# Kernel optimization log

Hardware: AMD Instinct MI355X
Metric: run time of the kernel (lower is better)

Reference implementation:

```python
import jax, jax.numpy as jnp
import numpy as np

EPS = 1e-6
ROPE_THETA = 10000.0


def setup_inputs() -> dict:
    key = jax.random.key(0)
    ks = jax.random.split(key, 6)
    B, S, D = 2, 2048, 2048
    H, KVH, HD = 16, 4, 128
    hidden_states = jax.random.normal(ks[0], (B, S, D), dtype=jnp.float32)
    # RoPE tables (HF style: freqs duplicated across the two halves)
    inv_freq = 1.0 / (ROPE_THETA ** (jnp.arange(0, HD, 2, dtype=jnp.float32) / HD))
    pos = jnp.arange(S, dtype=jnp.float32)
    freqs = pos[:, None] * inv_freq[None, :]            # [S, HD/2]
    emb = jnp.concatenate([freqs, freqs], axis=-1)       # [S, HD]
    cos, sin = jnp.cos(emb), jnp.sin(emb)
    w_scale = 0.02
    q_w = jax.random.normal(ks[1], (H * HD, D), dtype=jnp.float32) * w_scale
    k_w = jax.random.normal(ks[2], (KVH * HD, D), dtype=jnp.float32) * w_scale
    v_w = jax.random.normal(ks[3], (KVH * HD, D), dtype=jnp.float32) * w_scale
    o_w = jax.random.normal(ks[4], (D, H * HD), dtype=jnp.float32) * w_scale
    q_norm_w = jnp.ones((HD,), dtype=jnp.float32)
    k_norm_w = jnp.ones((HD,), dtype=jnp.float32)
    return {
        "hidden_states": hidden_states, "cos": cos, "sin": sin,
        "q_w": q_w, "k_w": k_w, "v_w": v_w, "o_w": o_w,
        "q_norm_w": q_norm_w, "k_norm_w": k_norm_w,
    }


def _rms_norm(x, w):
    # Qwen3RMSNorm: fp32 variance, scale, cast back
    xf = x.astype(jnp.float32)
    var = jnp.mean(xf * xf, axis=-1, keepdims=True)
    out = xf * jax.lax.rsqrt(var + EPS)
    return (out * w.astype(jnp.float32)).astype(x.dtype)


def _rotate_half(x):
    half = x.shape[-1] // 2
    return jnp.concatenate([-x[..., half:], x[..., :half]], axis=-1)


def reference(hidden_states, cos, sin, q_w, k_w, v_w, o_w, q_norm_w, k_norm_w):
    B, S, D = hidden_states.shape
    HD = q_norm_w.shape[0]
    H = q_w.shape[0] // HD
    KVH = k_w.shape[0] // HD
    groups = H // KVH
    scale = HD ** -0.5

    # QKV projections (no bias) -> [B, heads, S, HD]
    q = (hidden_states @ q_w.T).reshape(B, S, H, HD)
    k = (hidden_states @ k_w.T).reshape(B, S, KVH, HD)
    v = (hidden_states @ v_w.T).reshape(B, S, KVH, HD)
    q = _rms_norm(q, q_norm_w).transpose(0, 2, 1, 3)   # [B,H,S,HD]
    k = _rms_norm(k, k_norm_w).transpose(0, 2, 1, 3)   # [B,KVH,S,HD]
    v = v.transpose(0, 2, 1, 3)                        # [B,KVH,S,HD]

    # RoPE (broadcast over batch and heads)
    c = cos[None, None, :, :]
    s = sin[None, None, :, :]
    q = q * c + _rotate_half(q) * s
    k = k * c + _rotate_half(k) * s

    # GQA expand kv heads
    if groups > 1:
        k = jnp.repeat(k, groups, axis=1)              # [B,H,S,HD]
        v = jnp.repeat(v, groups, axis=1)

    # SDPA, non-causal, no mask, no dropout
    scores = jnp.einsum("bhqd,bhkd->bhqk", q, k) * scale
    probs = jax.nn.softmax(scores, axis=-1)
    attn = jnp.einsum("bhqk,bhkd->bhqd", probs, v)     # [B,H,S,HD]

    attn = attn.transpose(0, 2, 1, 3).reshape(B, S, H * HD)
    return attn @ o_w.T
```

## Files before the change

kernel.cpp:

```cpp
#include <hip/hip_runtime.h>
#include <hip/hip_bf16.h>
#include <math.h>

#define B_   2
#define S_   2048
#define D_   2048
#define H_   16
#define KVH_ 4
#define HD_  128
#define SCALE 0.08838834764831845f
#define LOG2E 1.44269504088896f
#define EPS_  1e-6f

typedef unsigned short u16;
typedef unsigned int   u32;
typedef __attribute__((ext_vector_type(2)))  unsigned int u32x2;
typedef __attribute__((ext_vector_type(8)))  short bf16x8;
typedef __attribute__((ext_vector_type(4)))  float f32x4;
typedef __attribute__((ext_vector_type(16))) float f32x16;

__device__ __forceinline__ u16 f2bf(float x) {
    union { float f; unsigned int u; } v; v.f = x;
    unsigned int r = v.u + 0x7fffu + ((v.u >> 16) & 1u);
    return (u16)(r >> 16);
}
__device__ __forceinline__ float bf2f(u16 b) {
    union { float f; unsigned int u; } v; v.u = ((unsigned int)b) << 16;
    return v.f;
}
__device__ __forceinline__ u32 cvtpk(float lo, float hi) {
    u32 r;
    asm("v_cvt_pk_bf16_f32 %0, %1, %2" : "=v"(r) : "v"(lo), "v"(hi));
    return r;
}
__device__ __forceinline__ void gload16(const void* g, void* lds) {
    __builtin_amdgcn_global_load_lds(
        (const __attribute__((address_space(1))) unsigned int*)g,
        (__attribute__((address_space(3))) unsigned int*)lds, 16, 0, 0);
}

__global__ __launch_bounds__(256) void f2b_all(
    const float* __restrict__ s0, u16* __restrict__ d0, int n0,
    const float* __restrict__ s1, u16* __restrict__ d1, int n1,
    const float* __restrict__ s2, u16* __restrict__ d2, int n2,
    const float* __restrict__ s3, u16* __restrict__ d3, int n3,
    const float* __restrict__ s4, u16* __restrict__ d4, int n4)
{
    const float* s; u16* d; int n;
    switch (blockIdx.y) {
        case 0: s = s0; d = d0; n = n0; break;
        case 1: s = s1; d = d1; n = n1; break;
        case 2: s = s2; d = d2; n = n2; break;
        case 3: s = s3; d = d3; n = n3; break;
        default: s = s4; d = d4; n = n4; break;
    }
    int i = blockIdx.x * 256 + threadIdx.x;
    if (i >= n) return;
    float4 v = ((const float4*)s)[i];
    ushort4 o = make_ushort4(f2bf(v.x), f2bf(v.y), f2bf(v.z), f2bf(v.w));
    ((ushort4*)d)[i] = o;
}

template<int MODE>
__global__ __launch_bounds__(256) void gemm_bf16(
    const u16* __restrict__ A,
    const u16* __restrict__ Bw,
    u16* __restrict__ Qo, u16* __restrict__ Ko, u16* __restrict__ Vt,
    float* __restrict__ Co)
{
    __shared__ u16 As[128 * 64];
    __shared__ u16 Bs[128 * 64];

    const int t  = threadIdx.x;
    const int w  = t >> 6, l = t & 63;
    const int wm = w >> 1, wn = w & 1;
    const int lr = l & 15, lh = l >> 4;
    const int n0 = blockIdx.x * 128;
    const int m0 = blockIdx.y * 128;

    f32x4 acc[4][4];
    #pragma unroll
    for (int i = 0; i < 4; ++i)
        #pragma unroll
        for (int j = 0; j < 4; ++j)
            acc[i][j] = (f32x4)0.f;

    const int x = (w * 4) * 1024 + l * 16;
    for (int k0 = 0; k0 < 2048; k0 += 64) {
        #pragma unroll
        for (int u = 0; u < 4; ++u) {
            int xb = x + u * 1024;
            int r  = xb >> 7;
            int c  = xb & 127;
            int cs = c ^ ((r & 7) << 4);
            gload16(&A[(size_t)(m0 + r) * 2048 + k0 + (cs >> 1)], &As[(w * 4 + u) * 512]);
            gload16(&Bw[(size_t)(n0 + r) * 2048 + k0 + (cs >> 1)], &Bs[(w * 4 + u) * 512]);
        }
        __syncthreads();
        #pragma unroll
        for (int kc = 0; kc < 2; ++kc) {
            bf16x8 af[4], bfr[4];
            #pragma unroll
            for (int i = 0; i < 4; ++i) {
                int row = wm * 64 + i * 16 + lr;
                int byt = row * 128 + ((kc * 64 + lh * 16) ^ ((row & 7) << 4));
                af[i] = *(const bf16x8*)&As[byt >> 1];
                int rob = wn * 64 + i * 16 + lr;
                int byb = rob * 128 + ((kc * 64 + lh * 16) ^ ((rob & 7) << 4));
                bfr[i] = *(const bf16x8*)&Bs[byb >> 1];
            }
            #pragma unroll
            for (int i = 0; i < 4; ++i)
                #pragma unroll
                for (int j = 0; j < 4; ++j)
                    acc[i][j] = __builtin_amdgcn_mfma_f32_16x16x32_bf16(
                        af[i], bfr[j], acc[i][j], 0, 0, 0);
        }
        __syncthreads();
    }

    #pragma unroll
    for (int i = 0; i < 4; ++i) {
        #pragma unroll
        for (int j = 0; j < 4; ++j) {
            int col = n0 + wn * 64 + j * 16 + lr;
            #pragma unroll
            for (int r = 0; r < 4; ++r) {
                int m = m0 + wm * 64 + i * 16 + lh * 4 + r;
                float v = acc[i][j][r];
                if (MODE == 0) {
                    int bb = m >> 11, s = m & 2047;
                    if (col < 2048) {
                        int hh = col >> 7, d = col & 127;
                        Qo[((size_t)(bb * H_ + hh) * S_ + s) * HD_ + d] = f2bf(v);
                    } else if (col < 2560) {
                        int c2 = col - 2048; int hh = c2 >> 7, d = c2 & 127;
                        Ko[((size_t)(bb * KVH_ + hh) * S_ + s) * HD_ + d] = f2bf(v);
                    } else {
                        int c2 = col - 2560; int hh = c2 >> 7, d = c2 & 127;
                        Vt[((size_t)(bb * KVH_ + hh) * HD_ + d) * S_ + s] = f2bf(v);
                    }
                } else {
                    Co[(size_t)m * 2048 + col] = v;
                }
            }
        }
    }
}

__global__ __launch_bounds__(256) void norm_rope(
    u16* __restrict__ Qb, u16* __restrict__ Kb,
    const float* __restrict__ cosb, const float* __restrict__ sinb,
    const float* __restrict__ qnw, const float* __restrict__ knw)
{
    const int rid = blockIdx.x * 4 + (threadIdx.x >> 6);
    const int l   = threadIdx.x & 63;
    u16* row; const float* wn; int s; float sc;
    if (rid < B_ * H_ * S_) {
        row = Qb + (size_t)rid * HD_; wn = qnw; s = rid & (S_ - 1); sc = SCALE * LOG2E;
    } else {
        int r2 = rid - B_ * H_ * S_;
        row = Kb + (size_t)r2 * HD_; wn = knw; s = r2 & (S_ - 1); sc = 1.f;
    }
    unsigned int u = *(const unsigned int*)&row[2 * l];
    float x0 = bf2f((u16)(u & 0xffff)), x1 = bf2f((u16)(u >> 16));
    float ss = x0 * x0 + x1 * x1;
    #pragma unroll
    for (int off = 1; off < 64; off <<= 1) ss += __shfl_xor(ss, off);
    float rr = rsqrtf(ss * (1.f / 128.f) + 1e-6f);
    float n0 = x0 * rr * wn[2 * l];
    float n1 = x1 * rr * wn[2 * l + 1];
    float p0 = __shfl_xor(n0, 32);
    float p1 = __shfl_xor(n1, 32);
    float sg = (l < 32) ? -1.f : 1.f;
    const float* cp = cosb + s * HD_;
    const float* sp = sinb + s * HD_;
    float o0 = (n0 * cp[2 * l]     + sg * p0 * sp[2 * l])     * sc;
    float o1 = (n1 * cp[2 * l + 1] + sg * p1 * sp[2 * l + 1]) * sc;
    unsigned int o = (unsigned int)f2bf(o0) | ((unsigned int)f2bf(o1) << 16);
    *(unsigned int*)&row[2 * l] = o;
}

__global__ __launch_bounds__(256, 2) void attn_mfma(
    const u16* __restrict__ Q,
    const u16* __restrict__ K,
    const u16* __restrict__ Vt,
    u16* __restrict__ AO)
{
    __shared__ u16 Ks[2][64 * 128];
    __shared__ u16 Vs[3][128 * 64];

    const int t  = threadIdx.x, w = t >> 6, l = t & 63;
    const int lq = l & 31, hi = l >> 5;
    const int id = (blockIdx.x & 7) * 64 + (blockIdx.x >> 3);
    const int qx = id & 15, bh = id >> 4;
    const int bb = bh >> 4, h = bh & 15;
    const int kv = bb * KVH_ + (h >> 2);
    const int q0 = qx * 128 + w * 32;

    const u16* Qp = Q + ((size_t)bh * S_ + q0) * HD_;
    const u16* Kp = K + (size_t)kv * S_ * HD_;
    const u16* Vp = Vt + (size_t)kv * HD_ * S_;

    bf16x8 aq[8];
    #pragma unroll
    for (int ks = 0; ks < 8; ++ks)
        aq[ks] = *(const bf16x8*)&Qp[(size_t)lq * 128 + ks * 16 + hi * 8];

    f32x16 oacc[4];
    #pragma unroll
    for (int dt = 0; dt < 4; ++dt) oacc[dt] = (f32x16)0.f;
    float mrun = -1e30f, lrun = 0.f;
    u32 pan[16];

    auto stage = [&](int k0, int kbuf, int vbuf) {
        #pragma unroll
        for (int u = 0; u < 4; ++u) {
            int xb = (w * 4 + u) * 1024 + l * 16;
            int rk = xb >> 8, ck = xb & 255;
            gload16(&Kp[(size_t)(k0 + rk) * 128 + ((ck ^ ((rk & 7) << 4)) >> 1)],
                    &Ks[kbuf][(w * 4 + u) * 512]);
            int rv = xb >> 7, cv = xb & 127;
            gload16(&Vp[(size_t)rv * S_ + k0 + ((cv ^ ((rv & 7) << 4)) >> 1)],
                    &Vs[vbuf][(w * 4 + u) * 512]);
        }
    };

    stage(0, 0, 0);
    __syncthreads();

    const int NT = S_ / 64;
    for (int kt = 0; kt < NT; ++kt) {
        const int kcur = kt & 1;
        if (kt + 1 < NT) stage((kt + 1) * 64, (kt + 1) & 1, (kt + 1) % 3);

        f32x16 sacc[2];
        sacc[0] = (f32x16)0.f; sacc[1] = (f32x16)0.f;
        #pragma unroll
        for (int kb = 0; kb < 2; ++kb) {
            #pragma unroll
            for (int ks = 0; ks < 8; ++ks) {
                int row = kb * 32 + lq;
                int byt = row * 256 + ((ks * 32 + hi * 16) ^ ((row & 7) << 4));
                bf16x8 kf = *(const bf16x8*)&Ks[kcur][byt >> 1];
                sacc[kb] = __builtin_amdgcn_mfma_f32_32x32x16_bf16(
                    kf, aq[ks], sacc[kb], 0, 0, 0);
            }
        }

        float mx = -1e30f;
        #pragma unroll
        for (int r = 0; r < 16; ++r)
            mx = fmaxf(mx, fmaxf(sacc[0][r], sacc[1][r]));
        mx = fmaxf(mx, __shfl_xor(mx, 32));

        if (kt > 0) {
            const int vprev = (kt + 2) % 3;
            #pragma unroll
            for (int g = 0; g < 4; ++g) {
                union { u32 u[4]; bf16x8 v; } pa;
                pa.u[0] = pan[g * 4 + 0]; pa.u[1] = pan[g * 4 + 1];
                pa.u[2] = pan[g * 4 + 2]; pa.u[3] = pan[g * 4 + 3];
                int kloc = g * 16 + hi * 8;
                #pragma unroll
                for (int dt = 0; dt < 4; ++dt) {
                    int rowv = dt * 32 + lq;
                    int byv  = rowv * 128 + ((kloc * 2) ^ ((rowv & 7) << 4));
                    bf16x8 vf = *(const bf16x8*)&Vs[vprev][byv >> 1];
                    oacc[dt] = __builtin_amdgcn_mfma_f32_32x32x16_bf16(
                        pa.v, vf, oacc[dt], 0, 0, 0);
                }
            }
        }

        if (__any(mx > mrun + 8.f)) {
            float mn = fmaxf(mrun, mx);
            float al = __builtin_exp2f(mrun - mn);
            mrun = mn;
            lrun *= al;
            #pragma unroll
            for (int r = 0; r < 16; ++r) {
                int src = (r & 3) + 8 * (r >> 2) + 4 * hi;
                float alr = __shfl(al, src);
                #pragma unroll
                for (int dt = 0; dt < 4; ++dt) oacc[dt][r] *= alr;
            }
        }

        float ps = 0.f;
        #pragma unroll
        for (int kb = 0; kb < 2; ++kb)
            #pragma unroll
            for (int r = 0; r < 16; ++r) {
                float p = __builtin_exp2f(sacc[kb][r] - mrun);
                sacc[kb][r] = p;
                ps += p;
            }
        ps += __shfl_xor(ps, 32);
        lrun += ps;

        #pragma unroll
        for (int kb = 0; kb < 2; ++kb) {
            u32 wv[8];
            #pragma unroll
            for (int i = 0; i < 8; ++i)
                wv[i] = cvtpk(sacc[kb][2 * i], sacc[kb][2 * i + 1]);
            #pragma unroll
            for (int k2 = 0; k2 < 2; ++k2) {
                u32x2 r0 = __builtin_amdgcn_permlane32_swap(
                    wv[4 * k2 + 0], wv[4 * k2 + 2], false, false);
                u32x2 r1 = __builtin_amdgcn_permlane32_swap(
                    wv[4 * k2 + 1], wv[4 * k2 + 3], false, false);
                int g = kb * 2 + k2;
                pan[g * 4 + 0] = r0.x; pan[g * 4 + 1] = r1.x;
                pan[g * 4 + 2] = r0.y; pan[g * 4 + 3] = r1.y;
            }
        }
        __syncthreads();
    }

    {
        const int vprev = (NT - 1) % 3;
        #pragma unroll
        for (int g = 0; g < 4; ++g) {
            union { u32 u[4]; bf16x8 v; } pa;
            pa.u[0] = pan[g * 4 + 0]; pa.u[1] = pan[g * 4 + 1];
            pa.u[2] = pan[g * 4 + 2]; pa.u[3] = pan[g * 4 + 3];
            int kloc = g * 16 + hi * 8;
            #pragma unroll
            for (int dt = 0; dt < 4; ++dt) {
                int rowv = dt * 32 + lq;
                int byv  = rowv * 128 + ((kloc * 2) ^ ((rowv & 7) << 4));
                bf16x8 vf = *(const bf16x8*)&Vs[vprev][byv >> 1];
                oacc[dt] = __builtin_amdgcn_mfma_f32_32x32x16_bf16(
                    pa.v, vf, oacc[dt], 0, 0, 0);
            }
        }
    }

    #pragma unroll
    for (int r = 0; r < 16; ++r) {
        int src = (r & 3) + 8 * (r >> 2) + 4 * hi;
        float linv = 1.f / __shfl(lrun, src);
        int s = q0 + src;
        size_t base = ((size_t)bb * S_ + s) * 2048 + h * 128 + lq;
        #pragma unroll
        for (int dt = 0; dt < 4; ++dt)
            AO[base + dt * 32] = f2bf(oacc[dt][r] * linv);
    }
}

extern "C" void kernel_launch(void* const* d_in, const int* in_sizes, int n_in,
                              void* d_out, int out_size, void* d_ws, size_t ws_size,
                              hipStream_t stream) {
    (void)in_sizes; (void)n_in; (void)out_size; (void)ws_size;
    const float* hid  = (const float*)d_in[0];
    const float* cosb = (const float*)d_in[1];
    const float* sinb = (const float*)d_in[2];
    const float* qw   = (const float*)d_in[3];
    const float* kw   = (const float*)d_in[4];
    const float* vw   = (const float*)d_in[5];
    const float* ow   = (const float*)d_in[6];
    const float* qnw  = (const float*)d_in[7];
    const float* knw  = (const float*)d_in[8];

    u16* ws   = (u16*)d_ws;
    u16* hidB = ws;
    u16* Wc   = ws + 8388608;
    u16* owB  = ws + 14680064;
    u16* Qb   = ws + 18874368;
    u16* Kb   = ws + 27262976;
    u16* VtB  = ws + 29360128;
    u16* AO   = ws + 31457280;

    f2b_all<<<dim3(8192, 5), 256, 0, stream>>>(
        hid, hidB, 2097152,
        qw,  Wc,            1048576,
        kw,  Wc + 4194304,  262144,
        vw,  Wc + 5242880,  262144,
        ow,  owB,           1048576);

    gemm_bf16<0><<<dim3(24, 32), 256, 0, stream>>>(hidB, Wc, Qb, Kb, VtB, nullptr);
    norm_rope<<<20480, 256, 0, stream>>>(Qb, Kb, cosb, sinb, qnw, knw);
    attn_mfma<<<512, 256, 0, stream>>>(Qb, Kb, VtB, AO);
    gemm_bf16<1><<<dim3(16, 32), 256, 0, stream>>>(AO, owB, nullptr, nullptr, nullptr,
                                                   (float*)d_out);
}
```

Baseline: 233.6 us.

## Fuse Q RMSNorm and RoPE into attention prologue; pack softmax ops

Q normalization and rotary embedding now run in the attention kernel's prologue on the Q fragments it loads into registers, so the norm kernel only handles K and launches 4096 blocks instead of 20480. This removes a full read-modify-write pass over the Q buffer in global memory. The attention inner loop also uses v_max3_f32 for the row max and packed v_pk_add_f32 for the max subtraction and the probability sum. The cost is extra prologue work and register pressure in the attention kernel, and the cos/sin loads per lane are not vectorized.

```diff
diff --git a/kernel.cpp b/kernel.cpp
--- a/kernel.cpp
+++ b/kernel.cpp
@@ -10,11 +10,13 @@
 #define HD_  128
 #define SCALE 0.08838834764831845f
 #define LOG2E 1.44269504088896f
+#define QSC_  (SCALE * LOG2E)
 #define EPS_  1e-6f
 
 typedef unsigned short u16;
 typedef unsigned int   u32;
 typedef __attribute__((ext_vector_type(2)))  unsigned int u32x2;
+typedef __attribute__((ext_vector_type(2)))  float f32x2;
 typedef __attribute__((ext_vector_type(8)))  short bf16x8;
 typedef __attribute__((ext_vector_type(4)))  float f32x4;
 typedef __attribute__((ext_vector_type(16))) float f32x16;
@@ -32,6 +34,17 @@
     u32 r;
     asm("v_cvt_pk_bf16_f32 %0, %1, %2" : "=v"(r) : "v"(lo), "v"(hi));
     return r;
+}
+__device__ __forceinline__ f32x2 pk_sub(f32x2 a, f32x2 b) {
+    f32x2 r;
+    asm("v_pk_add_f32 %0, %1, %2 neg_lo:[0,1] neg_hi:[0,1]" : "=v"(r) : "v"(a), "v"(b));
+    return r;
+}
+__device__ __forceinline__ f32x2 pk_add(f32x2 a, f32x2 b) {
+    f32x2 r; asm("v_pk_add_f32 %0, %1, %2" : "=v"(r) : "v"(a), "v"(b)); return r;
+}
+__device__ __forceinline__ float max3f(float a, float b, float c) {
+    float r; asm("v_max3_f32 %0, %1, %2, %3" : "=v"(r) : "v"(a), "v"(b), "v"(c)); return r;
 }
 __device__ __forceinline__ void gload16(const void* g, void* lds) {
     __builtin_amdgcn_global_load_lds(
@@ -148,35 +161,30 @@
     }
 }
 
-__global__ __launch_bounds__(256) void norm_rope(
-    u16* __restrict__ Qb, u16* __restrict__ Kb,
+__global__ __launch_bounds__(256) void norm_rope_k(
+    u16* __restrict__ Kb,
     const float* __restrict__ cosb, const float* __restrict__ sinb,
-    const float* __restrict__ qnw, const float* __restrict__ knw)
+    const float* __restrict__ knw)
 {
     const int rid = blockIdx.x * 4 + (threadIdx.x >> 6);
     const int l   = threadIdx.x & 63;
-    u16* row; const float* wn; int s; float sc;
-    if (rid < B_ * H_ * S_) {
-        row = Qb + (size_t)rid * HD_; wn = qnw; s = rid & (S_ - 1); sc = SCALE * LOG2E;
-    } else {
-        int r2 = rid - B_ * H_ * S_;
-        row = Kb + (size_t)r2 * HD_; wn = knw; s = r2 & (S_ - 1); sc = 1.f;
-    }
+    u16* row = Kb + (size_t)rid * HD_;
+    const int s  = rid & (S_ - 1);
     unsigned int u = *(const unsigned int*)&row[2 * l];
     float x0 = bf2f((u16)(u & 0xffff)), x1 = bf2f((u16)(u >> 16));
     float ss = x0 * x0 + x1 * x1;
     #pragma unroll
     for (int off = 1; off < 64; off <<= 1) ss += __shfl_xor(ss, off);
-    float rr = rsqrtf(ss * (1.f / 128.f) + 1e-6f);
-    float n0 = x0 * rr * wn[2 * l];
-    float n1 = x1 * rr * wn[2 * l + 1];
+    float rr = rsqrtf(ss * (1.f / 128.f) + EPS_);
+    float n0 = x0 * rr * knw[2 * l];
+    float n1 = x1 * rr * knw[2 * l + 1];
     float p0 = __shfl_xor(n0, 32);
     float p1 = __shfl_xor(n1, 32);
     float sg = (l < 32) ? -1.f : 1.f;
     const float* cp = cosb + s * HD_;
     const float* sp = sinb + s * HD_;
-    float o0 = (n0 * cp[2 * l]     + sg * p0 * sp[2 * l])     * sc;
-    float o1 = (n1 * cp[2 * l + 1] + sg * p1 * sp[2 * l + 1]) * sc;
+    float o0 = n0 * cp[2 * l]     + sg * p0 * sp[2 * l];
+    float o1 = n1 * cp[2 * l + 1] + sg * p1 * sp[2 * l + 1];
     unsigned int o = (unsigned int)f2bf(o0) | ((unsigned int)f2bf(o1) << 16);
     *(unsigned int*)&row[2 * l] = o;
 }
@@ -185,7 +193,9 @@
     const u16* __restrict__ Q,
     const u16* __restrict__ K,
     const u16* __restrict__ Vt,
-    u16* __restrict__ AO)
+    u16* __restrict__ AO,
+    const float* __restrict__ cosb, const float* __restrict__ sinb,
+    const float* __restrict__ qnw)
 {
     __shared__ u16 Ks[2][64 * 128];
     __shared__ u16 Vs[3][128 * 64];
@@ -203,9 +213,47 @@
     const u16* Vp = Vt + (size_t)kv * HD_ * S_;
 
     bf16x8 aq[8];
-    #pragma unroll
-    for (int ks = 0; ks < 8; ++ks)
-        aq[ks] = *(const bf16x8*)&Qp[(size_t)lq * 128 + ks * 16 + hi * 8];
+    {
+        bf16x8 raw[8];
+        #pragma unroll
+        for (int ks = 0; ks < 8; ++ks)
+            raw[ks] = *(const bf16x8*)&Qp[(size_t)lq * 128 + ks * 16 + hi * 8];
+        float ssq = 0.f;
+        #pragma unroll
+        for (int ks = 0; ks < 8; ++ks)
+            #pragma unroll
+            for (int e = 0; e < 8; ++e) {
+                float xv = bf2f((u16)raw[ks][e]); ssq += xv * xv;
+            }
+        ssq += __shfl_xor(ssq, 32);
+        float rr = rsqrtf(ssq * (1.f / 128.f) + EPS_);
+        const int srow = q0 + lq;
+        const float* cp = cosb + srow * HD_;
+        const float* sp = sinb + srow * HD_;
+        #pragma unroll
+        for (int ks = 0; ks < 4; ++ks) {
+            const int dlo = ks * 16 + hi * 8;
+            const int dhi = dlo + 64;
+            float olo[8], ohi[8];
+            #pragma unroll
+            for (int e = 0; e < 8; ++e) {
+                float nlo = bf2f((u16)raw[ks][e])     * rr * qnw[dlo + e];
+                float nhi = bf2f((u16)raw[ks + 4][e]) * rr * qnw[dhi + e];
+                float c0 = cp[dlo + e] * QSC_, s0 = sp[dlo + e] * QSC_;
+                float c1 = cp[dhi + e] * QSC_, s1 = sp[dhi + e] * QSC_;
+                olo[e] = nlo * c0 - nhi * s0;
+                ohi[e] = nhi * c1 + nlo * s1;
+            }
+            union { u32 u[4]; bf16x8 v; } plo, phi;
+            #pragma unroll
+            for (int e2 = 0; e2 < 4; ++e2) {
+                plo.u[e2] = cvtpk(olo[2 * e2], olo[2 * e2 + 1]);
+                phi.u[e2] = cvtpk(ohi[2 * e2], ohi[2 * e2 + 1]);
+            }
+            aq[ks]     = plo.v;
+            aq[ks + 4] = phi.v;
+        }
+    }
 
     f32x16 oacc[4];
     #pragma unroll
@@ -248,10 +296,14 @@
             }
         }
 
-        float mx = -1e30f;
-        #pragma unroll
-        for (int r = 0; r < 16; ++r)
-            mx = fmaxf(mx, fmaxf(sacc[0][r], sacc[1][r]));
+        float mxa = max3f(sacc[0][0], sacc[0][1], sacc[0][2]);
+        float mxb = max3f(sacc[1][0], sacc[1][1], sacc[1][2]);
+        #pragma unroll
+        for (int r = 3; r < 15; r += 2) {
+            mxa = max3f(mxa, sacc[0][r], sacc[0][r + 1]);
+            mxb = max3f(mxb, sacc[1][r], sacc[1][r + 1]);
+        }
+        float mx = max3f(fmaxf(mxa, sacc[0][15]), mxb, sacc[1][15]);
         mx = fmaxf(mx, __shfl_xor(mx, 32));
 
         if (kt > 0) {
@@ -287,15 +339,21 @@
             }
         }
 
-        float ps = 0.f;
-        #pragma unroll
-        for (int kb = 0; kb < 2; ++kb)
-            #pragma unroll
-            for (int r = 0; r < 16; ++r) {
-                float p = __builtin_exp2f(sacc[kb][r] - mrun);
-                sacc[kb][r] = p;
-                ps += p;
-            }
+        f32x2 mr2; mr2.x = mrun; mr2.y = mrun;
+        f32x2 ps2; ps2.x = 0.f; ps2.y = 0.f;
+        #pragma unroll
+        for (int kb = 0; kb < 2; ++kb) {
+            f32x2* s2 = (f32x2*)&sacc[kb];
+            #pragma unroll
+            for (int i = 0; i < 8; ++i) {
+                f32x2 dv = pk_sub(s2[i], mr2);
+                dv.x = __builtin_exp2f(dv.x);
+                dv.y = __builtin_exp2f(dv.y);
+                s2[i] = dv;
+                ps2 = pk_add(ps2, dv);
+            }
+        }
+        float ps = ps2.x + ps2.y;
         ps += __shfl_xor(ps, 32);
         lrun += ps;
 
@@ -381,8 +439,8 @@
         ow,  owB,           1048576);
 
     gemm_bf16<0><<<dim3(24, 32), 256, 0, stream>>>(hidB, Wc, Qb, Kb, VtB, nullptr);
-    norm_rope<<<20480, 256, 0, stream>>>(Qb, Kb, cosb, sinb, qnw, knw);
-    attn_mfma<<<512, 256, 0, stream>>>(Qb, Kb, VtB, AO);
+    norm_rope_k<<<4096, 256, 0, stream>>>(Kb, cosb, sinb, knw);
+    attn_mfma<<<512, 256, 0, stream>>>(Qb, Kb, VtB, AO, cosb, sinb, qnw);
     gemm_bf16<1><<<dim3(16, 32), 256, 0, stream>>>(AO, owB, nullptr, nullptr, nullptr,
                                                    (float*)d_out);
 }
```

Result: no change. 231.5 us (-0.9%).
